# Performance work log

Measured on AMD Instinct MI355X. Metric: run time of the kernel, lower is better.

Reference implementation:

```python
import jax, jax.numpy as jnp
import numpy as np

B, T, D = 4, 2048, 1024
H = 16
HD = D // H  # 64


def setup_inputs() -> dict:
    key = jax.random.key(0)
    ks = jax.random.split(key, 6)
    s = 0.02
    x = jax.random.normal(ks[0], (B, T, D), dtype=jnp.float32)
    # per-head projection weights, stored stacked: [H, HD, D] (torch Linear weight layout)
    Wq = jax.random.normal(ks[1], (H, HD, D), dtype=jnp.float32) * s
    Wk = jax.random.normal(ks[2], (H, HD, D), dtype=jnp.float32) * s
    Wv = jax.random.normal(ks[3], (H, HD, D), dtype=jnp.float32) * s
    Wo = jax.random.normal(ks[4], (D, D), dtype=jnp.float32) * s  # proj weight [out, in]
    bo = jax.random.normal(ks[5], (D,), dtype=jnp.float32) * s
    return {"x": x, "Wq": Wq, "Wk": Wk, "Wv": Wv, "Wo": Wo, "bo": bo}


def reference(x, Wq, Wk, Wv, Wo, bo):
    Bx, Tx, _ = x.shape
    # project: [B,T,D] x [H,HD,D] -> [B,H,T,HD]
    q = jnp.einsum('btd,hed->bhte', x, Wq)
    k = jnp.einsum('btd,hed->bhte', x, Wk)
    v = jnp.einsum('btd,hed->bhte', x, Wv)
    scale = 1.0 / jnp.sqrt(jnp.array(q.shape[-1], dtype=x.dtype))
    scores = jnp.einsum('bhte,bhse->bhts', q, k) * scale  # [B,H,T,T]
    causal = jnp.tril(jnp.ones((Tx, Tx), dtype=bool))
    scores = jnp.where(causal, scores, jnp.array(-jnp.inf, dtype=scores.dtype))
    weights = jax.nn.softmax(scores, axis=-1)
    out = jnp.einsum('bhts,bhse->bhte', weights, v)  # [B,H,T,HD]
    # concat heads (head h occupies contiguous slice, matching torch.cat order)
    out = out.transpose(0, 2, 1, 3).reshape(Bx, Tx, -1)  # [B,T,D]
    out = out @ Wo.T + bo
    return out
```

## Files before the change

### kernel.cpp

```cpp
#include <hip/hip_runtime.h>
#include <cstdint>
#include <cstddef>

typedef unsigned short u16;
typedef float  f32x4  __attribute__((ext_vector_type(4)));
typedef __bf16 bf16x8 __attribute__((ext_vector_type(8)));
typedef unsigned short us8 __attribute__((ext_vector_type(8)));
typedef unsigned short us4 __attribute__((ext_vector_type(4)));
typedef float  f32x4v __attribute__((ext_vector_type(4)));
typedef unsigned int u32x2 __attribute__((ext_vector_type(2)));

#define AS1 __attribute__((address_space(1)))
#define AS3 __attribute__((address_space(3)))

__device__ __forceinline__ u16 f2b(float f) {
  unsigned u = __float_as_uint(f);
  u += 0x7FFFu + ((u >> 16) & 1u);
  return (u16)(u >> 16);
}

__device__ __forceinline__ unsigned pkbf(float a, float b) {
  unsigned ua = __float_as_uint(a) + 0x8000u;
  unsigned ub = __float_as_uint(b) + 0x8000u;
  return __builtin_amdgcn_perm(ub, ua, 0x07060302u);
}

__device__ __forceinline__ unsigned cvtpk(float a, float b) {
  unsigned short lo = __builtin_bit_cast(unsigned short, (__bf16)a);
  unsigned short hi = __builtin_bit_cast(unsigned short, (__bf16)b);
  return (unsigned)lo | ((unsigned)hi << 16);
}

__device__ __forceinline__ bf16x8 ldfrag(const u16* p) {
  us8 v = *(const us8*)p;
  return __builtin_bit_cast(bf16x8, v);
}

__device__ __forceinline__ f32x4 mfma16(bf16x8 a, bf16x8 b, f32x4 c) {
  return __builtin_amdgcn_mfma_f32_16x16x32_bf16(a, b, c, 0, 0, 0);
}

__device__ __forceinline__ void gl_lds16(const u16* g, AS3 u16* l) {
  __builtin_amdgcn_global_load_lds((AS1 void*)g, (AS3 void*)l, 16, 0, 0);
}


__global__ __launch_bounds__(256) void cvt_all(
    const float* __restrict__ x,
    const float* __restrict__ Wq, const float* __restrict__ Wk,
    const float* __restrict__ Wv, const float* __restrict__ Wo,
    u16* __restrict__ xb, u16* __restrict__ Wqkv, u16* __restrict__ Wob) {
  for (int blk = blockIdx.x; blk < 12288; blk += 3072) {
    const float* s;
    u16* d;
    int i;
    if (blk < 8192)       { s = x;  d = xb;             i = blk * 256 + threadIdx.x; }
    else if (blk < 9216)  { s = Wq; d = Wqkv;           i = (blk - 8192) * 256 + threadIdx.x; }
    else if (blk < 10240) { s = Wk; d = Wqkv + 1048576; i = (blk - 9216) * 256 + threadIdx.x; }
    else if (blk < 11264) { s = Wv; d = Wqkv + 2097152; i = (blk - 10240) * 256 + threadIdx.x; }
    else                  { s = Wo; d = Wob;            i = (blk - 11264) * 256 + threadIdx.x; }
    f32x4v f = ((const f32x4v*)s)[i];
    us4 o = { f2b(f[0]), f2b(f[1]), f2b(f[2]), f2b(f[3]) };
    ((us4*)d)[i] = o;
  }
}

__global__ __launch_bounds__(256) void gemm_qkv(
    const u16* __restrict__ A, const u16* __restrict__ W,
    u16* __restrict__ Qb, u16* __restrict__ Kb, u16* __restrict__ Vt) {
  __shared__ u16 lA[128 * 64];
  __shared__ u16 lB[128 * 64];
  const int tid = threadIdx.x;
  const int lane = tid & 63, wave = tid >> 6;
  const int quad = lane >> 4, l16 = lane & 15;
  const int wr = wave >> 1, wc = wave & 1;

  const int p = blockIdx.x;
  const int l = (p & 7) * 64 + (p >> 3);
  const int by = l >> 3;
  const int bx0 = l & 7;
  const int m0 = by * 128;

  AS3 u16* lA3 = (AS3 u16*)lA;
  AS3 u16* lB3 = (AS3 u16*)lB;
  const int g3 = (((lane & 7) ^ (lane >> 3)) * 8);
  const int srow = lane >> 3;
  const int pA = ((quad) ^ (l16 & 7)) * 8;
  const int pB = ((4 + quad) ^ (l16 & 7)) * 8;

  const u16* gA = A + (size_t)(m0 + wave * 8 + srow) * 1024 + g3;

#pragma unroll 1
  for (int sec = 0; sec < 3; sec++) {
    const int n0 = (bx0 + sec * 8) * 128;
    const u16* gB = W + (size_t)(n0 + wave * 8 + srow) * 1024 + g3;
    f32x4 acc[4][4] = {};

    for (int k0 = 0; k0 < 1024; k0 += 64) {
      __syncthreads();
#pragma unroll
      for (int i = 0; i < 4; i++) {
        gl_lds16(gA + (size_t)i * 32768 + k0, lA3 + (i * 4 + wave) * 512);
        gl_lds16(gB + (size_t)i * 32768 + k0, lB3 + (i * 4 + wave) * 512);
      }
      __syncthreads();
#pragma unroll
      for (int kk = 0; kk < 2; kk++) {
        const int pk = kk ? pB : pA;
        bf16x8 aF[4], bF[4];
#pragma unroll
        for (int mt = 0; mt < 4; mt++)
          aF[mt] = ldfrag(&lA[(wr * 64 + mt * 16 + l16) * 64 + pk]);
#pragma unroll
        for (int nt = 0; nt < 4; nt++)
          bF[nt] = ldfrag(&lB[(wc * 64 + nt * 16 + l16) * 64 + pk]);
        if (sec != 2) {
#pragma unroll
          for (int mt = 0; mt < 4; mt++)
#pragma unroll
            for (int nt = 0; nt < 4; nt++)
              acc[mt][nt] = mfma16(bF[nt], aF[mt], acc[mt][nt]);
        } else {
#pragma unroll
          for (int mt = 0; mt < 4; mt++)
#pragma unroll
            for (int nt = 0; nt < 4; nt++)
              acc[mt][nt] = mfma16(aF[mt], bF[nt], acc[mt][nt]);
        }
      }
    }

    if (sec != 2) {
      const float qsc = (sec == 0) ? 0.180336880111120426f : 1.0f;
      u16* __restrict__ D = (sec == 0) ? Qb : Kb;
      const int hb = ((n0 & 1023) >> 6) + wc;
#pragma unroll
      for (int mt = 0; mt < 4; mt++) {
        int t = m0 + wr * 64 + mt * 16 + l16;
        int b = t >> 11, tt = t & 2047;
        size_t rowb = (((size_t)b * 16 + hb) * 2048 + tt) * 64;
#pragma unroll
        for (int nt = 0; nt < 4; nt++) {
          int e = nt * 16 + quad * 4;
          u32x2 pk = { pkbf(acc[mt][nt][0] * qsc, acc[mt][nt][1] * qsc),
                       pkbf(acc[mt][nt][2] * qsc, acc[mt][nt][3] * qsc) };
          *(u32x2*)&D[rowb + e] = pk;
        }
      }
    } else {
#pragma unroll
      for (int mt = 0; mt < 4; mt++) {
        int t = m0 + wr * 64 + mt * 16 + quad * 4;
        int b = t >> 11, tt = t & 2047;
#pragma unroll
        for (int nt = 0; nt < 4; nt++) {
          int ns = (n0 & 1023) + wc * 64 + nt * 16 + l16;
          int h = ns >> 6, e = ns & 63;
          size_t addr = (((size_t)b * 16 + h) * 64 + e) * 2048 + tt;
          u32x2 pk = { pkbf(acc[mt][nt][0], acc[mt][nt][1]),
                       pkbf(acc[mt][nt][2], acc[mt][nt][3]) };
          *(u32x2*)&Vt[addr] = pk;
        }
      }
    }
  }
}

__global__ __launch_bounds__(512, 4) void attn(
    const u16* __restrict__ Q, const u16* __restrict__ K,
    const u16* __restrict__ Vt, u16* __restrict__ O) {
  __shared__ u16 lK[256 * 64];
  __shared__ u16 lV[64 * 256];
  __shared__ u16 lP[8 * 16 * 40];
  const int tid = threadIdx.x;
  const int lane = tid & 63, wave = tid >> 6;
  const int quad = lane >> 4, l16 = lane & 15;
  const int bh = blockIdx.x;
  const int pidx = blockIdx.y;
  const size_t base = (size_t)bh * (2048 * 64);
  u16* lPw = lP + wave * 640;
  const int b = bh >> 4, h = bh & 15;
  AS3 u16* lK3 = (AS3 u16*)lK;
  AS3 u16* lV3 = (AS3 u16*)lV;

  const int g3 = ((lane & 7) ^ (lane >> 3)) * 8;
  const u16* gK0 = K + base + (size_t)(tid >> 3) * 64 + g3;
  const int gcV = (((tid & 31) ^ ((tid >> 5) & 7)) * 8);
  const u16* gV0 = Vt + base + (size_t)(tid >> 5) * 2048 + gcV;

  const int e7 = l16 & 7;
  const int pq0 = (quad ^ e7) * 8;
  const int pq1 = ((4 + quad) ^ e7) * 8;

  us8 ones_u = { 0x3F80, 0x3F80, 0x3F80, 0x3F80, 0x3F80, 0x3F80, 0x3F80, 0x3F80 };
  const bf16x8 onesA = __builtin_bit_cast(bf16x8, ones_u);

  for (int half = 0; half < 2; half++) {
    const int qb = half ? pidx : (15 - pidx);
    const int t0 = qb << 7;
    const int tq = t0 + wave * 16 + l16;
    const bf16x8 qF0 = ldfrag(Q + base + (size_t)tq * 64 + quad * 8);
    const bf16x8 qF1 = ldfrag(Q + base + (size_t)tq * 64 + 32 + quad * 8);
    float l_i = 0.f;
    f32x4 o[4] = {};
    const int niter = (qb + 2) >> 1;

    for (int j = 0; j < niter; j++) {
      const int s0 = j << 8;
      __syncthreads();
#pragma unroll
      for (int i = 0; i < 4; i++) {
        gl_lds16(gK0 + (size_t)(s0 + i * 64) * 64, lK3 + i * 4096 + wave * 512);
        gl_lds16(gV0 + (size_t)i * 32768 + s0,     lV3 + i * 4096 + wave * 512);
      }
      __syncthreads();

#pragma unroll
      for (int hh = 0; hh < 2; hh++) {
        const int s0h = s0 + hh * 128;
        if (s0h > t0) break;

        f32x4 S[8];
        __builtin_amdgcn_s_setprio(1);
#pragma unroll
        for (int nt = 0; nt < 8; nt++) {
          int sr = hh * 128 + nt * 16 + l16;
          f32x4 a = {};
          a = mfma16(ldfrag(&lK[sr * 64 + pq0]), qF0, a);
          a = mfma16(ldfrag(&lK[sr * 64 + pq1]), qF1, a);
          S[nt] = a;
        }
        __builtin_amdgcn_s_setprio(0);

        if (s0h == t0) {
#pragma unroll
          for (int nt = 0; nt < 8; nt++)
#pragma unroll
            for (int r = 0; r < 4; r++) {
              int s = s0h + nt * 16 + quad * 4 + r;
              if (s > tq) S[nt][r] = -INFINITY;
            }
        }

#pragma unroll
        for (int nt = 0; nt < 8; nt++)
#pragma unroll
          for (int r = 0; r < 4; r++)
            S[nt][r] = __builtin_amdgcn_exp2f(S[nt][r]);

        f32x4 ol = {};
#pragma unroll
        for (int c = 0; c < 4; c++) {
          u32x2 d0 = { cvtpk(S[2*c][0],   S[2*c][1]),   cvtpk(S[2*c][2],   S[2*c][3]) };
          u32x2 d1 = { cvtpk(S[2*c+1][0], S[2*c+1][1]), cvtpk(S[2*c+1][2], S[2*c+1][3]) };
          *(u32x2*)&lPw[l16 * 40 + quad * 4]      = d0;
          *(u32x2*)&lPw[l16 * 40 + 16 + quad * 4] = d1;
          __asm__ volatile("s_waitcnt lgkmcnt(0)" ::: "memory");
          bf16x8 bP = ldfrag(&lPw[l16 * 40 + quad * 8]);
          __builtin_amdgcn_s_setprio(1);
#pragma unroll
          for (int ot = 0; ot < 4; ot++) {
            int pos = ((hh * 16 + c * 4 + quad) ^ e7) * 8;
            o[ot] = mfma16(ldfrag(&lV[(ot * 16 + l16) * 256 + pos]), bP, o[ot]);
          }
          ol = mfma16(onesA, bP, ol);
          __builtin_amdgcn_s_setprio(0);
        }
        l_i += ol[0];
      }
    }

    const float inv = 1.f / l_i;
#pragma unroll
    for (int ot = 0; ot < 4; ot++) {
      u32x2 pk = { cvtpk(o[ot][0] * inv, o[ot][1] * inv),
                   cvtpk(o[ot][2] * inv, o[ot][3] * inv) };
      *(u32x2*)&O[((size_t)b * 2048 + tq) * 1024 + h * 64 + ot * 16 + quad * 4] = pk;
    }
  }
}

__global__ __launch_bounds__(256) void gemm_out(
    const u16* __restrict__ A, const u16* __restrict__ W,
    const float* __restrict__ bias, float* __restrict__ out) {
  __shared__ u16 lA[128 * 64];
  __shared__ u16 lB[128 * 64];
  const int tid = threadIdx.x;
  const int lane = tid & 63, wave = tid >> 6;
  const int quad = lane >> 4, l16 = lane & 15;
  const int wr = wave >> 1, wc = wave & 1;
  const int m0 = blockIdx.y * 128;
  const int n0 = blockIdx.x * 128;
  AS3 u16* lA3 = (AS3 u16*)lA;
  AS3 u16* lB3 = (AS3 u16*)lB;
  f32x4 acc[4][4] = {};
  const int g3 = (((lane & 7) ^ (lane >> 3)) * 8);
  const int srow = lane >> 3;
  const int pA = ((quad) ^ (l16 & 7)) * 8;
  const int pB = ((4 + quad) ^ (l16 & 7)) * 8;
  const u16* gA = A + (size_t)(m0 + wave * 8 + srow) * 1024 + g3;
  const u16* gB = W + (size_t)(n0 + wave * 8 + srow) * 1024 + g3;

  for (int k0 = 0; k0 < 1024; k0 += 64) {
    __syncthreads();
#pragma unroll
    for (int i = 0; i < 4; i++) {
      gl_lds16(gA + (size_t)i * 32768 + k0, lA3 + (i * 4 + wave) * 512);
      gl_lds16(gB + (size_t)i * 32768 + k0, lB3 + (i * 4 + wave) * 512);
    }
    __syncthreads();
#pragma unroll
    for (int kk = 0; kk < 2; kk++) {
      const int pk = kk ? pB : pA;
      bf16x8 aF[4], bF[4];
#pragma unroll
      for (int mt = 0; mt < 4; mt++)
        aF[mt] = ldfrag(&lA[(wr * 64 + mt * 16 + l16) * 64 + pk]);
#pragma unroll
      for (int nt = 0; nt < 4; nt++)
        bF[nt] = ldfrag(&lB[(wc * 64 + nt * 16 + l16) * 64 + pk]);
#pragma unroll
      for (int mt = 0; mt < 4; mt++)
#pragma unroll
        for (int nt = 0; nt < 4; nt++)
          acc[mt][nt] = mfma16(aF[mt], bF[nt], acc[mt][nt]);
    }
  }

#pragma unroll
  for (int mt = 0; mt < 4; mt++) {
#pragma unroll
    for (int nt = 0; nt < 4; nt++) {
#pragma unroll
      for (int r = 0; r < 4; r++) {
        int m = m0 + wr * 64 + mt * 16 + quad * 4 + r;
        int n = n0 + wc * 64 + nt * 16 + l16;
        out[(size_t)m * 1024 + n] = acc[mt][nt][r] + bias[n];
      }
    }
  }
}

extern "C" void kernel_launch(void* const* d_in, const int* in_sizes, int n_in,
                              void* d_out, int out_size, void* d_ws, size_t ws_size,
                              hipStream_t stream) {
  const float* x  = (const float*)d_in[0];
  const float* Wq = (const float*)d_in[1];
  const float* Wk = (const float*)d_in[2];
  const float* Wv = (const float*)d_in[3];
  const float* Wo = (const float*)d_in[4];
  const float* bo = (const float*)d_in[5];
  float* out = (float*)d_out;

  u16* ws   = (u16*)d_ws;
  u16* xb   = ws;
  u16* Wqkv = ws + 8388608;
  u16* Wob  = ws + 11534336;
  u16* Qb   = ws + 12582912;
  u16* Ao   = xb;
  u16* Kb   = (u16*)d_out;
  u16* Vt   = Kb + 8388608;

  cvt_all<<<3072, 256, 0, stream>>>(x, Wq, Wk, Wv, Wo, xb, Wqkv, Wob);
  gemm_qkv<<<512, 256, 0, stream>>>(xb, Wqkv, Qb, Kb, Vt);
  attn<<<dim3(64, 8), 512, 0, stream>>>(Qb, Kb, Vt, Ao);
  gemm_out<<<dim3(8, 64), 256, 0, stream>>>(Ao, Wob, bo, out);
}
```

Measured before the change: 237.3 us.

## Process both paired query blocks in one pass over shared K/V tiles

```diff
diff --git a/kernel.cpp b/kernel.cpp
--- a/kernel.cpp
+++ b/kernel.cpp
@@ -195,87 +195,96 @@
   us8 ones_u = { 0x3F80, 0x3F80, 0x3F80, 0x3F80, 0x3F80, 0x3F80, 0x3F80, 0x3F80 };
   const bf16x8 onesA = __builtin_bit_cast(bf16x8, ones_u);
 
-  for (int half = 0; half < 2; half++) {
-    const int qb = half ? pidx : (15 - pidx);
-    const int t0 = qb << 7;
-    const int tq = t0 + wave * 16 + l16;
-    const bf16x8 qF0 = ldfrag(Q + base + (size_t)tq * 64 + quad * 8);
-    const bf16x8 qF1 = ldfrag(Q + base + (size_t)tq * 64 + 32 + quad * 8);
-    float l_i = 0.f;
-    f32x4 o[4] = {};
-    const int niter = (qb + 2) >> 1;
-
-    for (int j = 0; j < niter; j++) {
-      const int s0 = j << 8;
-      __syncthreads();
-#pragma unroll
-      for (int i = 0; i < 4; i++) {
-        gl_lds16(gK0 + (size_t)(s0 + i * 64) * 64, lK3 + i * 4096 + wave * 512);
-        gl_lds16(gV0 + (size_t)i * 32768 + s0,     lV3 + i * 4096 + wave * 512);
-      }
-      __syncthreads();
-
-#pragma unroll
-      for (int hh = 0; hh < 2; hh++) {
-        const int s0h = s0 + hh * 128;
-        if (s0h > t0) break;
-
-        f32x4 S[8];
-        __builtin_amdgcn_s_setprio(1);
-#pragma unroll
-        for (int nt = 0; nt < 8; nt++) {
-          int sr = hh * 128 + nt * 16 + l16;
-          f32x4 a = {};
-          a = mfma16(ldfrag(&lK[sr * 64 + pq0]), qF0, a);
-          a = mfma16(ldfrag(&lK[sr * 64 + pq1]), qF1, a);
-          S[nt] = a;
-        }
-        __builtin_amdgcn_s_setprio(0);
-
-        if (s0h == t0) {
-#pragma unroll
-          for (int nt = 0; nt < 8; nt++)
-#pragma unroll
-            for (int r = 0; r < 4; r++) {
-              int s = s0h + nt * 16 + quad * 4 + r;
-              if (s > tq) S[nt][r] = -INFINITY;
-            }
-        }
-
-#pragma unroll
-        for (int nt = 0; nt < 8; nt++)
-#pragma unroll
-          for (int r = 0; r < 4; r++)
-            S[nt][r] = __builtin_amdgcn_exp2f(S[nt][r]);
-
-        f32x4 ol = {};
-#pragma unroll
-        for (int c = 0; c < 4; c++) {
-          u32x2 d0 = { cvtpk(S[2*c][0],   S[2*c][1]),   cvtpk(S[2*c][2],   S[2*c][3]) };
-          u32x2 d1 = { cvtpk(S[2*c+1][0], S[2*c+1][1]), cvtpk(S[2*c+1][2], S[2*c+1][3]) };
-          *(u32x2*)&lPw[l16 * 40 + quad * 4]      = d0;
-          *(u32x2*)&lPw[l16 * 40 + 16 + quad * 4] = d1;
-          __asm__ volatile("s_waitcnt lgkmcnt(0)" ::: "memory");
-          bf16x8 bP = ldfrag(&lPw[l16 * 40 + quad * 8]);
-          __builtin_amdgcn_s_setprio(1);
-#pragma unroll
-          for (int ot = 0; ot < 4; ot++) {
-            int pos = ((hh * 16 + c * 4 + quad) ^ e7) * 8;
-            o[ot] = mfma16(ldfrag(&lV[(ot * 16 + l16) * 256 + pos]), bP, o[ot]);
-          }
-          ol = mfma16(onesA, bP, ol);
-          __builtin_amdgcn_s_setprio(0);
-        }
-        l_i += ol[0];
-      }
-    }
-
-    const float inv = 1.f / l_i;
+  const int qbL = 15 - pidx, qbH = pidx;
+  const int t0L = qbL << 7,  t0H = qbH << 7;
+  const int tqL = t0L + wave * 16 + l16;
+  const int tqH = t0H + wave * 16 + l16;
+  const bf16x8 qF0L = ldfrag(Q + base + (size_t)tqL * 64 + quad * 8);
+  const bf16x8 qF1L = ldfrag(Q + base + (size_t)tqL * 64 + 32 + quad * 8);
+  const bf16x8 qF0H = ldfrag(Q + base + (size_t)tqH * 64 + quad * 8);
+  const bf16x8 qF1H = ldfrag(Q + base + (size_t)tqH * 64 + 32 + quad * 8);
+  float lL = 0.f, lH = 0.f;
+  f32x4 oL[4] = {}, oH[4] = {};
+  const int niter = (qbL + 2) >> 1;
+
+#define ATTN_HALF(tq_, t0_, qf0_, qf1_, o_, l_) do {                         \
+    f32x4 S[8];                                                              \
+    __builtin_amdgcn_s_setprio(1);                                           \
+    _Pragma("unroll") for (int nt = 0; nt < 8; nt++) {                       \
+      int sr = hh * 128 + nt * 16 + l16;                                     \
+      f32x4 a = {};                                                          \
+      a = mfma16(ldfrag(&lK[sr * 64 + pq0]), qf0_, a);                       \
+      a = mfma16(ldfrag(&lK[sr * 64 + pq1]), qf1_, a);                       \
+      S[nt] = a;                                                             \
+    }                                                                        \
+    __builtin_amdgcn_s_setprio(0);                                           \
+    if (s0h == t0_) {                                                        \
+      _Pragma("unroll") for (int nt = 0; nt < 8; nt++)                       \
+      _Pragma("unroll") for (int r = 0; r < 4; r++) {                        \
+        int s = s0h + nt * 16 + quad * 4 + r;                                \
+        if (s > tq_) S[nt][r] = -INFINITY;                                   \
+      }                                                                      \
+    }                                                                        \
+    _Pragma("unroll") for (int nt = 0; nt < 8; nt++)                         \
+    _Pragma("unroll") for (int r = 0; r < 4; r++)                            \
+      S[nt][r] = __builtin_amdgcn_exp2f(S[nt][r]);                           \
+    f32x4 ol = {};                                                           \
+    _Pragma("unroll") for (int c = 0; c < 4; c++) {                          \
+      u32x2 d0 = { cvtpk(S[2*c][0],   S[2*c][1]),   cvtpk(S[2*c][2],   S[2*c][3]) };   \
+      u32x2 d1 = { cvtpk(S[2*c+1][0], S[2*c+1][1]), cvtpk(S[2*c+1][2], S[2*c+1][3]) }; \
+      *(u32x2*)&lPw[l16 * 40 + quad * 4]      = d0;                          \
+      *(u32x2*)&lPw[l16 * 40 + 16 + quad * 4] = d1;                          \
+      __asm__ volatile("s_waitcnt lgkmcnt(0)" ::: "memory");                 \
+      bf16x8 bP = ldfrag(&lPw[l16 * 40 + quad * 8]);                         \
+      __builtin_amdgcn_s_setprio(1);                                         \
+      _Pragma("unroll") for (int ot = 0; ot < 4; ot++) {                     \
+        int pos = ((hh * 16 + c * 4 + quad) ^ e7) * 8;                       \
+        o_[ot] = mfma16(ldfrag(&lV[(ot * 16 + l16) * 256 + pos]), bP, o_[ot]); \
+      }                                                                      \
+      ol = mfma16(onesA, bP, ol);                                            \
+      __builtin_amdgcn_s_setprio(0);                                         \
+    }                                                                        \
+    l_ += ol[0];                                                             \
+  } while (0)
+
+#pragma unroll 1
+  for (int j = 0; j < niter; j++) {
+    const int s0 = j << 8;
+    __syncthreads();
+#pragma unroll
+    for (int i = 0; i < 4; i++) {
+      gl_lds16(gK0 + (size_t)(s0 + i * 64) * 64, lK3 + i * 4096 + wave * 512);
+      gl_lds16(gV0 + (size_t)i * 32768 + s0,     lV3 + i * 4096 + wave * 512);
+    }
+    __syncthreads();
+
+#pragma unroll
+    for (int hh = 0; hh < 2; hh++) {
+      const int s0h = s0 + hh * 128;
+      if (s0h > t0L) break;
+      ATTN_HALF(tqL, t0L, qF0L, qF1L, oL, lL);
+      if (s0h <= t0H)
+        ATTN_HALF(tqH, t0H, qF0H, qF1H, oH, lH);
+    }
+  }
+#undef ATTN_HALF
+
+  {
+    const float inv = 1.f / lL;
 #pragma unroll
     for (int ot = 0; ot < 4; ot++) {
-      u32x2 pk = { cvtpk(o[ot][0] * inv, o[ot][1] * inv),
-                   cvtpk(o[ot][2] * inv, o[ot][3] * inv) };
-      *(u32x2*)&O[((size_t)b * 2048 + tq) * 1024 + h * 64 + ot * 16 + quad * 4] = pk;
+      u32x2 pk = { cvtpk(oL[ot][0] * inv, oL[ot][1] * inv),
+                   cvtpk(oL[ot][2] * inv, oL[ot][3] * inv) };
+      *(u32x2*)&O[((size_t)b * 2048 + tqL) * 1024 + h * 64 + ot * 16 + quad * 4] = pk;
+    }
+  }
+  {
+    const float inv = 1.f / lH;
+#pragma unroll
+    for (int ot = 0; ot < 4; ot++) {
+      u32x2 pk = { cvtpk(oH[ot][0] * inv, oH[ot][1] * inv),
+                   cvtpk(oH[ot][2] * inv, oH[ot][3] * inv) };
+      *(u32x2*)&O[((size_t)b * 2048 + tqH) * 1024 + h * 64 + ot * 16 + quad * 4] = pk;
     }
   }
 }
```

After: 239.0 us. About the same (+0.7%).
